# Kernel tuning notes

Measured on AMD Instinct MI355X. Metric: run time of the kernel, lower is better.

Reference implementation:

```python
import jax, jax.numpy as jnp
import numpy as np

W = 4           # cp_size (simulated ranks)
NUM_HEADS = 32
HEAD_SIZE = 128
NUM_KV_HEADS = 8
BLOCK_SIZE = 16
NUM_BLOCKS = 1024
MAX_BLOCKS = 32
MAX_CTX = 512   # <= _PARTITION_SIZE so single-partition stats are exact
NUM_SEQS = 32
SCALE = 1.0 / np.sqrt(HEAD_SIZE)
NEG_INF = -1e30


def setup_inputs() -> dict:
    key = jax.random.key(0)
    k1, k2, k3, k4, k5 = jax.random.split(key, 5)
    query = jax.random.normal(k1, (NUM_SEQS, 1, NUM_HEADS * HEAD_SIZE), dtype=jnp.float32)
    # per-rank paged KV caches, layout [W, num_blocks, kv_heads, block_size, head_size]
    key_cache = jax.random.normal(k2, (W, NUM_BLOCKS, NUM_KV_HEADS, BLOCK_SIZE, HEAD_SIZE), dtype=jnp.float32)
    value_cache = jax.random.normal(k3, (W, NUM_BLOCKS, NUM_KV_HEADS, BLOCK_SIZE, HEAD_SIZE), dtype=jnp.float32)
    block_tables = jax.random.randint(k4, (W, NUM_SEQS, MAX_BLOCKS), 0, NUM_BLOCKS, dtype=jnp.int32)
    context_lens = jax.random.randint(k5, (W, NUM_SEQS), 1, MAX_CTX + 1, dtype=jnp.int32)
    return {"query": query, "key_cache": key_cache, "value_cache": value_cache,
            "block_tables": block_tables, "context_lens": context_lens}


def reference(query, key_cache, value_cache, block_tables, context_lens):
    B, L, _ = query.shape
    S = B * L                       # num_seqs (decode: L=1)
    G = NUM_KV_HEADS
    Q = NUM_HEADS // G              # queries per kv head
    T = MAX_BLOCKS * BLOCK_SIZE     # max context per rank

    q = query.reshape(S, G, Q, HEAD_SIZE)
    ridx = jnp.arange(W)[:, None, None]
    # gather paged blocks: [W, S, MAX_BLOCKS, G, BLOCK_SIZE, D] -> [W, S, G, T, D]
    k = key_cache[ridx, block_tables].transpose(0, 1, 3, 2, 4, 5).reshape(W, S, G, T, HEAD_SIZE)
    v = value_cache[ridx, block_tables].transpose(0, 1, 3, 2, 4, 5).reshape(W, S, G, T, HEAD_SIZE)

    logits = jnp.einsum('sgqd,wsgtd->wsgqt', q, k) * SCALE
    mask = jnp.arange(T)[None, None, None, None, :] < context_lens[:, :, None, None, None]
    logits = jnp.where(mask, logits, NEG_INF)

    # per-rank online-softmax stats (== paged_attention_v2 single-partition output)
    m = jnp.max(logits, axis=-1)                      # [W,S,G,Q] max logit per rank
    p = jnp.exp(logits - m[..., None])
    p = jnp.where(mask, p, 0.0)
    esum = jnp.sum(p, axis=-1)                        # [W,S,G,Q]
    out_r = jnp.einsum('wsgqt,wsgtd->wsgqd', p, v) / esum[..., None]  # normalized per-rank out

    # cross-rank log-sum-exp reduction (distributed_paged_attention_v2_reduce)
    gmax = jnp.max(m, axis=0)                         # [S,G,Q]
    w_r = esum * jnp.exp(m - gmax[None])              # [W,S,G,Q]
    out = jnp.sum(out_r * w_r[..., None], axis=0) / jnp.sum(w_r, axis=0)[..., None]

    return out.reshape(B, L, NUM_HEADS * HEAD_SIZE)
```

## Files before the change

### kernel.cpp

```cpp
#include <hip/hip_runtime.h>
#include <math.h>

#define W 4
#define NUM_HEADS 32
#define HEAD_SIZE 128
#define G 8
#define QPG 4
#define BLOCK_SZ 16
#define NUM_BLOCKS 1024
#define MAX_BLOCKS 32
#define S 32
#define SPLIT 2
#define NPART (W * SPLIT)
#define SCALE 0.08838834764831845f
#define NEG_BIG (-1e30f)

#define BLK_STRIDE (G * BLOCK_SZ * HEAD_SIZE)
#define WG_STRIDE  (NUM_BLOCKS * BLK_STRIDE)

__global__ __launch_bounds__(256, 5)
void pa_partial_kernel(const float* __restrict__ query,
                       const float* __restrict__ key_cache,
                       const float* __restrict__ value_cache,
                       const int* __restrict__ block_tables,
                       const int* __restrict__ context_lens,
                       float* __restrict__ acc_ws,
                       float* __restrict__ m_ws,
                       float* __restrict__ e_ws)
{
    int bx = blockIdx.x;
    const int p = bx % SPLIT; bx /= SPLIT;
    const int g = bx % G;     bx /= G;
    const int s = bx % S;
    const int w = bx / S;

    const int tid   = threadIdx.x;
    const int accid = tid >> 5;
    const int lane  = tid & 31;
    const int d0    = lane * 4;
    const int h     = accid + 8 * p;

    __shared__ int   bt_lds[MAX_BLOCKS];
    __shared__ float sm_m[8][QPG];
    __shared__ float sm_e[8][QPG];
    __shared__ float sm_acc[8][QPG][HEAD_SIZE];

    if (tid < MAX_BLOCKS)
        bt_lds[tid] = block_tables[((size_t)w * S + s) * MAX_BLOCKS + tid];
    __syncthreads();

    float4 qf[QPG];
#pragma unroll
    for (int qi = 0; qi < QPG; ++qi)
        qf[qi] = *reinterpret_cast<const float4*>(
            query + ((size_t)s * NUM_HEADS + g * QPG + qi) * HEAD_SIZE + d0);

    const int ctx = context_lens[w * S + s];
    const float* kbase = key_cache   + (size_t)w * WG_STRIDE + (size_t)g * BLOCK_SZ * HEAD_SIZE;
    const float* vbase = value_cache + (size_t)w * WG_STRIDE + (size_t)g * BLOCK_SZ * HEAD_SIZE;

    float  m_i[QPG], e_i[QPG];
    float4 acc[QPG];
#pragma unroll
    for (int qi = 0; qi < QPG; ++qi) {
        m_i[qi] = NEG_BIG; e_i[qi] = 0.f;
        acc[qi] = make_float4(0.f, 0.f, 0.f, 0.f);
    }

    for (int t = h; t < ctx; t += 2 * 16) {
        const int off1 = bt_lds[t >> 4] * BLK_STRIDE + (t & 15) * HEAD_SIZE + d0;
        const float4 k1 = *reinterpret_cast<const float4*>(kbase + off1);
        const float4 v1 = *reinterpret_cast<const float4*>(vbase + off1);
        const int  t2   = t + 16;
        const bool vld2 = t2 < ctx;
        float4 k2 = make_float4(0.f, 0.f, 0.f, 0.f);
        float4 v2 = make_float4(0.f, 0.f, 0.f, 0.f);
        if (vld2) {
            const int off2 = bt_lds[t2 >> 4] * BLK_STRIDE + (t2 & 15) * HEAD_SIZE + d0;
            k2 = *reinterpret_cast<const float4*>(kbase + off2);
            v2 = *reinterpret_cast<const float4*>(vbase + off2);
        }

        float4 dv1, dv2;
        dv1.x = qf[0].x*k1.x + qf[0].y*k1.y + qf[0].z*k1.z + qf[0].w*k1.w;
        dv1.y = qf[1].x*k1.x + qf[1].y*k1.y + qf[1].z*k1.z + qf[1].w*k1.w;
        dv1.z = qf[2].x*k1.x + qf[2].y*k1.y + qf[2].z*k1.z + qf[2].w*k1.w;
        dv1.w = qf[3].x*k1.x + qf[3].y*k1.y + qf[3].z*k1.z + qf[3].w*k1.w;
        dv2.x = qf[0].x*k2.x + qf[0].y*k2.y + qf[0].z*k2.z + qf[0].w*k2.w;
        dv2.y = qf[1].x*k2.x + qf[1].y*k2.y + qf[1].z*k2.z + qf[1].w*k2.w;
        dv2.z = qf[2].x*k2.x + qf[2].y*k2.y + qf[2].z*k2.z + qf[2].w*k2.w;
        dv2.w = qf[3].x*k2.x + qf[3].y*k2.y + qf[3].z*k2.z + qf[3].w*k2.w;
#pragma unroll
        for (int o = 16; o > 0; o >>= 1) {
            dv1.x += __shfl_xor(dv1.x, o); dv1.y += __shfl_xor(dv1.y, o);
            dv1.z += __shfl_xor(dv1.z, o); dv1.w += __shfl_xor(dv1.w, o);
            dv2.x += __shfl_xor(dv2.x, o); dv2.y += __shfl_xor(dv2.y, o);
            dv2.z += __shfl_xor(dv2.z, o); dv2.w += __shfl_xor(dv2.w, o);
        }
        const float l1[QPG] = {dv1.x*SCALE, dv1.y*SCALE, dv1.z*SCALE, dv1.w*SCALE};
        float l2[QPG] = {dv2.x*SCALE, dv2.y*SCALE, dv2.z*SCALE, dv2.w*SCALE};
#pragma unroll
        for (int qi = 0; qi < QPG; ++qi) if (!vld2) l2[qi] = NEG_BIG;

#pragma unroll
        for (int qi = 0; qi < QPG; ++qi) {
            const float mn    = fmaxf(m_i[qi], fmaxf(l1[qi], l2[qi]));
            const float alpha = __expf(m_i[qi] - mn);
            const float p1    = __expf(l1[qi] - mn);
            const float p2    = __expf(l2[qi] - mn);
            m_i[qi] = mn;
            e_i[qi] = e_i[qi] * alpha + (p1 + p2);
            acc[qi].x = fmaf(acc[qi].x, alpha, fmaf(p1, v1.x, p2 * v2.x));
            acc[qi].y = fmaf(acc[qi].y, alpha, fmaf(p1, v1.y, p2 * v2.y));
            acc[qi].z = fmaf(acc[qi].z, alpha, fmaf(p1, v1.z, p2 * v2.z));
            acc[qi].w = fmaf(acc[qi].w, alpha, fmaf(p1, v1.w, p2 * v2.w));
        }
    }

#pragma unroll
    for (int qi = 0; qi < QPG; ++qi) {
        if (lane == 0) { sm_m[accid][qi] = m_i[qi]; sm_e[accid][qi] = e_i[qi]; }
        sm_acc[accid][qi][d0 + 0] = acc[qi].x;
        sm_acc[accid][qi][d0 + 1] = acc[qi].y;
        sm_acc[accid][qi][d0 + 2] = acc[qi].z;
        sm_acc[accid][qi][d0 + 3] = acc[qi].w;
    }
    __syncthreads();

    const int r = w * SPLIT + p;
    for (int pi = tid; pi < QPG * HEAD_SIZE; pi += 256) {
        const int qi = pi >> 7;
        const int d  = pi & (HEAD_SIZE - 1);
        float gm = NEG_BIG;
#pragma unroll
        for (int hh = 0; hh < 8; ++hh) gm = fmaxf(gm, sm_m[hh][qi]);
        float num = 0.f, den = 0.f;
#pragma unroll
        for (int hh = 0; hh < 8; ++hh) {
            const float sc = __expf(sm_m[hh][qi] - gm);
            num += sm_acc[hh][qi][d] * sc;
            den += sm_e[hh][qi] * sc;
        }
        const size_t idx = (((size_t)r * S + s) * G + g) * QPG + qi;
        acc_ws[idx * HEAD_SIZE + d] = num;
        if (d == 0) { m_ws[idx] = gm; e_ws[idx] = den; }
    }
}

__global__ __launch_bounds__(256)
void pa_reduce_kernel(const float* __restrict__ acc_ws,
                      const float* __restrict__ m_ws,
                      const float* __restrict__ e_ws,
                      float* __restrict__ out)
{
    const int bx = blockIdx.x;
    const int s = bx / G, g = bx % G;
    const int tid = threadIdx.x;
    for (int pi = tid; pi < QPG * HEAD_SIZE; pi += 256) {
        const int qi = pi >> 7;
        const int d  = pi & (HEAD_SIZE - 1);
        float mw[NPART], ew[NPART];
        float gm = NEG_BIG;
#pragma unroll
        for (int r = 0; r < NPART; ++r) {
            const size_t idx = (((size_t)r * S + s) * G + g) * QPG + qi;
            mw[r] = m_ws[idx];
            ew[r] = e_ws[idx];
            gm = fmaxf(gm, mw[r]);
        }
        float num = 0.f, den = 0.f;
#pragma unroll
        for (int r = 0; r < NPART; ++r) {
            const float sc = __expf(mw[r] - gm);
            const size_t idx = (((size_t)r * S + s) * G + g) * QPG + qi;
            num += acc_ws[idx * HEAD_SIZE + d] * sc;
            den += ew[r] * sc;
        }
        out[((size_t)s * NUM_HEADS + g * QPG + qi) * HEAD_SIZE + d] = num / den;
    }
}

__global__ __launch_bounds__(256)
void pa_fused_kernel(const float* __restrict__ query,
                     const float* __restrict__ key_cache,
                     const float* __restrict__ value_cache,
                     const int* __restrict__ block_tables,
                     const int* __restrict__ context_lens,
                     float* __restrict__ out)
{
    const int bx = blockIdx.x;
    const int s = bx / G, g = bx % G;
    const int tid   = threadIdx.x;
    const int accid = tid >> 5;
    const int lane  = tid & 31;
    const int d0    = lane * 4;

    __shared__ int   bt_lds[MAX_BLOCKS];
    __shared__ float sm_m[8][QPG];
    __shared__ float sm_e[8][QPG];
    __shared__ float sm_acc[8][QPG][HEAD_SIZE];

    float4 qf[QPG];
#pragma unroll
    for (int qi = 0; qi < QPG; ++qi)
        qf[qi] = *reinterpret_cast<const float4*>(
            query + ((size_t)s * NUM_HEADS + g * QPG + qi) * HEAD_SIZE + d0);

    float  m_i[QPG], e_i[QPG];
    float4 acc[QPG];
#pragma unroll
    for (int qi = 0; qi < QPG; ++qi) {
        m_i[qi] = NEG_BIG; e_i[qi] = 0.f;
        acc[qi] = make_float4(0.f, 0.f, 0.f, 0.f);
    }

    for (int w = 0; w < W; ++w) {
        __syncthreads();
        if (tid < MAX_BLOCKS)
            bt_lds[tid] = block_tables[((size_t)w * S + s) * MAX_BLOCKS + tid];
        __syncthreads();
        const int ctx = context_lens[w * S + s];
        const float* kbase = key_cache   + (size_t)w * WG_STRIDE + (size_t)g * BLOCK_SZ * HEAD_SIZE;
        const float* vbase = value_cache + (size_t)w * WG_STRIDE + (size_t)g * BLOCK_SZ * HEAD_SIZE;
        for (int t = accid; t < ctx; t += 8) {
            const int off = bt_lds[t >> 4] * BLK_STRIDE + (t & 15) * HEAD_SIZE + d0;
            const float4 kx = *reinterpret_cast<const float4*>(kbase + off);
            const float4 vx = *reinterpret_cast<const float4*>(vbase + off);
            float4 dv;
            dv.x = qf[0].x*kx.x + qf[0].y*kx.y + qf[0].z*kx.z + qf[0].w*kx.w;
            dv.y = qf[1].x*kx.x + qf[1].y*kx.y + qf[1].z*kx.z + qf[1].w*kx.w;
            dv.z = qf[2].x*kx.x + qf[2].y*kx.y + qf[2].z*kx.z + qf[2].w*kx.w;
            dv.w = qf[3].x*kx.x + qf[3].y*kx.y + qf[3].z*kx.z + qf[3].w*kx.w;
#pragma unroll
            for (int o = 16; o > 0; o >>= 1) {
                dv.x += __shfl_xor(dv.x, o); dv.y += __shfl_xor(dv.y, o);
                dv.z += __shfl_xor(dv.z, o); dv.w += __shfl_xor(dv.w, o);
            }
            const float lg[QPG] = {dv.x*SCALE, dv.y*SCALE, dv.z*SCALE, dv.w*SCALE};
#pragma unroll
            for (int qi = 0; qi < QPG; ++qi) {
                const float mn    = fmaxf(m_i[qi], lg[qi]);
                const float alpha = __expf(m_i[qi] - mn);
                const float pp    = __expf(lg[qi] - mn);
                m_i[qi] = mn;
                e_i[qi] = e_i[qi] * alpha + pp;
                acc[qi].x = fmaf(acc[qi].x, alpha, pp * vx.x);
                acc[qi].y = fmaf(acc[qi].y, alpha, pp * vx.y);
                acc[qi].z = fmaf(acc[qi].z, alpha, pp * vx.z);
                acc[qi].w = fmaf(acc[qi].w, alpha, pp * vx.w);
            }
        }
    }

#pragma unroll
    for (int qi = 0; qi < QPG; ++qi) {
        if (lane == 0) { sm_m[accid][qi] = m_i[qi]; sm_e[accid][qi] = e_i[qi]; }
        sm_acc[accid][qi][d0 + 0] = acc[qi].x;
        sm_acc[accid][qi][d0 + 1] = acc[qi].y;
        sm_acc[accid][qi][d0 + 2] = acc[qi].z;
        sm_acc[accid][qi][d0 + 3] = acc[qi].w;
    }
    __syncthreads();

    for (int pi = tid; pi < QPG * HEAD_SIZE; pi += 256) {
        const int qi = pi >> 7;
        const int d  = pi & (HEAD_SIZE - 1);
        float gm = NEG_BIG;
#pragma unroll
        for (int hh = 0; hh < 8; ++hh) gm = fmaxf(gm, sm_m[hh][qi]);
        float num = 0.f, den = 0.f;
#pragma unroll
        for (int hh = 0; hh < 8; ++hh) {
            const float sc = __expf(sm_m[hh][qi] - gm);
            num += sm_acc[hh][qi][d] * sc;
            den += sm_e[hh][qi] * sc;
        }
        out[((size_t)s * NUM_HEADS + g * QPG + qi) * HEAD_SIZE + d] = num / den;
    }
}

extern "C" void kernel_launch(void* const* d_in, const int* in_sizes, int n_in,
                              void* d_out, int out_size, void* d_ws, size_t ws_size,
                              hipStream_t stream) {
    const float* query        = (const float*)d_in[0];
    const float* key_cache    = (const float*)d_in[1];
    const float* value_cache  = (const float*)d_in[2];
    const int*   block_tables = (const int*)d_in[3];
    const int*   context_lens = (const int*)d_in[4];
    float* out = (float*)d_out;

    const size_t n_acc   = (size_t)NPART * S * G * QPG * HEAD_SIZE;
    const size_t n_stats = (size_t)NPART * S * G * QPG;
    const size_t need    = (n_acc + 2 * n_stats) * sizeof(float);

    if (ws_size >= need) {
        float* acc_ws = (float*)d_ws;
        float* m_ws   = acc_ws + n_acc;
        float* e_ws   = m_ws + n_stats;
        pa_partial_kernel<<<W * S * G * SPLIT, 256, 0, stream>>>(
            query, key_cache, value_cache, block_tables, context_lens,
            acc_ws, m_ws, e_ws);
        pa_reduce_kernel<<<S * G, 256, 0, stream>>>(acc_ws, m_ws, e_ws, out);
    } else {
        pa_fused_kernel<<<S * G, 256, 0, stream>>>(
            query, key_cache, value_cache, block_tables, context_lens, out);
    }
}
```

Before: 463.7 us.

## Double-buffer KV chunks in LDS via async global_load_lds in partial kernel

The partial attention kernel now stages each 16-token KV block for its head into shared memory with the asynchronous global-to-LDS load builtin, double-buffered so the next block's load overlaps compute on the current one. Partition assignment changes from interleaved tokens to interleaved whole blocks per split, and the accumulator scratch reuses the staging buffer. This aims to hide global load latency and issue wider coalesced loads, at the cost of more LDS (32KB), a barrier per chunk, and occupancy lowered from 5 to 4 blocks per CU.

```diff
diff --git a/kernel.cpp b/kernel.cpp
--- a/kernel.cpp
+++ b/kernel.cpp
@@ -1,5 +1,6 @@
 #include <hip/hip_runtime.h>
 #include <math.h>
+#include <stdint.h>
 
 #define W 4
 #define NUM_HEADS 32
@@ -16,9 +17,27 @@
 #define NEG_BIG (-1e30f)
 
 #define BLK_STRIDE (G * BLOCK_SZ * HEAD_SIZE)
-#define WG_STRIDE  (NUM_BLOCKS * BLK_STRIDE)
-
-__global__ __launch_bounds__(256, 5)
+#define WG_STRIDE  ((size_t)NUM_BLOCKS * BLK_STRIDE)
+#define CHUNK_ELEMS (BLOCK_SZ * HEAD_SIZE)
+
+typedef const __attribute__((address_space(1))) uint32_t* gas_ptr;
+typedef __attribute__((address_space(3))) uint32_t* las_ptr;
+
+__device__ __forceinline__ void stage_chunk(const float* __restrict__ ksrc,
+                                            const float* __restrict__ vsrc,
+                                            float* kv_dst, int tid)
+{
+    const int wv = tid >> 6;
+    const int ln = tid & 63;
+    const int b0 = wv * 512;
+    const int b1 = b0 + 256;
+    __builtin_amdgcn_global_load_lds((gas_ptr)(ksrc + b0 + ln * 4), (las_ptr)(kv_dst + b0),               16, 0, 0);
+    __builtin_amdgcn_global_load_lds((gas_ptr)(ksrc + b1 + ln * 4), (las_ptr)(kv_dst + b1),               16, 0, 0);
+    __builtin_amdgcn_global_load_lds((gas_ptr)(vsrc + b0 + ln * 4), (las_ptr)(kv_dst + CHUNK_ELEMS + b0), 16, 0, 0);
+    __builtin_amdgcn_global_load_lds((gas_ptr)(vsrc + b1 + ln * 4), (las_ptr)(kv_dst + CHUNK_ELEMS + b1), 16, 0, 0);
+}
+
+__global__ __launch_bounds__(256, 4)
 void pa_partial_kernel(const float* __restrict__ query,
                        const float* __restrict__ key_cache,
                        const float* __restrict__ value_cache,
@@ -29,8 +48,8 @@
                        float* __restrict__ e_ws)
 {
     int bx = blockIdx.x;
-    const int p = bx % SPLIT; bx /= SPLIT;
-    const int g = bx % G;     bx /= G;
+    const int p = bx & 1; bx >>= 1;
+    const int g = bx % G; bx /= G;
     const int s = bx % S;
     const int w = bx / S;
 
@@ -38,16 +57,16 @@
     const int accid = tid >> 5;
     const int lane  = tid & 31;
     const int d0    = lane * 4;
-    const int h     = accid + 8 * p;
-
-    __shared__ int   bt_lds[MAX_BLOCKS];
-    __shared__ float sm_m[8][QPG];
-    __shared__ float sm_e[8][QPG];
-    __shared__ float sm_acc[8][QPG][HEAD_SIZE];
-
-    if (tid < MAX_BLOCKS)
-        bt_lds[tid] = block_tables[((size_t)w * S + s) * MAX_BLOCKS + tid];
-    __syncthreads();
+
+    __shared__ float smem[2 * 2 * CHUNK_ELEMS];
+    __shared__ float sm_m[8][QPG], sm_e[8][QPG];
+
+    const int ctx    = context_lens[w * S + s];
+    const int nc_all = (ctx + BLOCK_SZ - 1) >> 4;
+    const int cnt    = (nc_all - p + 1) >> 1;
+    const int* bt = block_tables + ((size_t)w * S + s) * MAX_BLOCKS;
+    const float* kbase = key_cache   + (size_t)w * WG_STRIDE + (size_t)g * CHUNK_ELEMS;
+    const float* vbase = value_cache + (size_t)w * WG_STRIDE + (size_t)g * CHUNK_ELEMS;
 
     float4 qf[QPG];
 #pragma unroll
@@ -55,10 +74,6 @@
         qf[qi] = *reinterpret_cast<const float4*>(
             query + ((size_t)s * NUM_HEADS + g * QPG + qi) * HEAD_SIZE + d0);
 
-    const int ctx = context_lens[w * S + s];
-    const float* kbase = key_cache   + (size_t)w * WG_STRIDE + (size_t)g * BLOCK_SZ * HEAD_SIZE;
-    const float* vbase = value_cache + (size_t)w * WG_STRIDE + (size_t)g * BLOCK_SZ * HEAD_SIZE;
-
     float  m_i[QPG], e_i[QPG];
     float4 acc[QPG];
 #pragma unroll
@@ -67,63 +82,77 @@
         acc[qi] = make_float4(0.f, 0.f, 0.f, 0.f);
     }
 
-    for (int t = h; t < ctx; t += 2 * 16) {
-        const int off1 = bt_lds[t >> 4] * BLK_STRIDE + (t & 15) * HEAD_SIZE + d0;
-        const float4 k1 = *reinterpret_cast<const float4*>(kbase + off1);
-        const float4 v1 = *reinterpret_cast<const float4*>(vbase + off1);
-        const int  t2   = t + 16;
-        const bool vld2 = t2 < ctx;
-        float4 k2 = make_float4(0.f, 0.f, 0.f, 0.f);
-        float4 v2 = make_float4(0.f, 0.f, 0.f, 0.f);
-        if (vld2) {
-            const int off2 = bt_lds[t2 >> 4] * BLK_STRIDE + (t2 & 15) * HEAD_SIZE + d0;
-            k2 = *reinterpret_cast<const float4*>(kbase + off2);
-            v2 = *reinterpret_cast<const float4*>(vbase + off2);
-        }
-
-        float4 dv1, dv2;
-        dv1.x = qf[0].x*k1.x + qf[0].y*k1.y + qf[0].z*k1.z + qf[0].w*k1.w;
-        dv1.y = qf[1].x*k1.x + qf[1].y*k1.y + qf[1].z*k1.z + qf[1].w*k1.w;
-        dv1.z = qf[2].x*k1.x + qf[2].y*k1.y + qf[2].z*k1.z + qf[2].w*k1.w;
-        dv1.w = qf[3].x*k1.x + qf[3].y*k1.y + qf[3].z*k1.z + qf[3].w*k1.w;
-        dv2.x = qf[0].x*k2.x + qf[0].y*k2.y + qf[0].z*k2.z + qf[0].w*k2.w;
-        dv2.y = qf[1].x*k2.x + qf[1].y*k2.y + qf[1].z*k2.z + qf[1].w*k2.w;
-        dv2.z = qf[2].x*k2.x + qf[2].y*k2.y + qf[2].z*k2.z + qf[2].w*k2.w;
-        dv2.w = qf[3].x*k2.x + qf[3].y*k2.y + qf[3].z*k2.z + qf[3].w*k2.w;
-#pragma unroll
-        for (int o = 16; o > 0; o >>= 1) {
-            dv1.x += __shfl_xor(dv1.x, o); dv1.y += __shfl_xor(dv1.y, o);
-            dv1.z += __shfl_xor(dv1.z, o); dv1.w += __shfl_xor(dv1.w, o);
-            dv2.x += __shfl_xor(dv2.x, o); dv2.y += __shfl_xor(dv2.y, o);
-            dv2.z += __shfl_xor(dv2.z, o); dv2.w += __shfl_xor(dv2.w, o);
-        }
-        const float l1[QPG] = {dv1.x*SCALE, dv1.y*SCALE, dv1.z*SCALE, dv1.w*SCALE};
-        float l2[QPG] = {dv2.x*SCALE, dv2.y*SCALE, dv2.z*SCALE, dv2.w*SCALE};
-#pragma unroll
-        for (int qi = 0; qi < QPG; ++qi) if (!vld2) l2[qi] = NEG_BIG;
-
-#pragma unroll
-        for (int qi = 0; qi < QPG; ++qi) {
-            const float mn    = fmaxf(m_i[qi], fmaxf(l1[qi], l2[qi]));
-            const float alpha = __expf(m_i[qi] - mn);
-            const float p1    = __expf(l1[qi] - mn);
-            const float p2    = __expf(l2[qi] - mn);
-            m_i[qi] = mn;
-            e_i[qi] = e_i[qi] * alpha + (p1 + p2);
-            acc[qi].x = fmaf(acc[qi].x, alpha, fmaf(p1, v1.x, p2 * v2.x));
-            acc[qi].y = fmaf(acc[qi].y, alpha, fmaf(p1, v1.y, p2 * v2.y));
-            acc[qi].z = fmaf(acc[qi].z, alpha, fmaf(p1, v1.z, p2 * v2.z));
-            acc[qi].w = fmaf(acc[qi].w, alpha, fmaf(p1, v1.w, p2 * v2.w));
-        }
-    }
-
+    if (cnt > 0) {
+        const size_t bb = (size_t)bt[p] * BLK_STRIDE;
+        stage_chunk(kbase + bb, vbase + bb, smem, tid);
+    }
+    __syncthreads();
+
+    int buf = 0;
+    for (int i = 0; i < cnt; ++i) {
+        const int c = p + 2 * i;
+        if (i + 1 < cnt) {
+            const size_t bb = (size_t)bt[c + 2] * BLK_STRIDE;
+            stage_chunk(kbase + bb, vbase + bb, smem + (buf ^ 1) * (2 * CHUNK_ELEMS), tid);
+        }
+
+        const float* kb = smem + buf * (2 * CHUNK_ELEMS);
+        const float* vb = kb + CHUNK_ELEMS;
+        const int gt0 = (c << 4) + accid;
+        if (gt0 < ctx) {
+            const float4 k1 = *reinterpret_cast<const float4*>(kb + accid * HEAD_SIZE + d0);
+            const float4 v1 = *reinterpret_cast<const float4*>(vb + accid * HEAD_SIZE + d0);
+            const float4 k2 = *reinterpret_cast<const float4*>(kb + (accid + 8) * HEAD_SIZE + d0);
+            const float4 v2 = *reinterpret_cast<const float4*>(vb + (accid + 8) * HEAD_SIZE + d0);
+
+            float4 dv1, dv2;
+            dv1.x = qf[0].x*k1.x + qf[0].y*k1.y + qf[0].z*k1.z + qf[0].w*k1.w;
+            dv1.y = qf[1].x*k1.x + qf[1].y*k1.y + qf[1].z*k1.z + qf[1].w*k1.w;
+            dv1.z = qf[2].x*k1.x + qf[2].y*k1.y + qf[2].z*k1.z + qf[2].w*k1.w;
+            dv1.w = qf[3].x*k1.x + qf[3].y*k1.y + qf[3].z*k1.z + qf[3].w*k1.w;
+            dv2.x = qf[0].x*k2.x + qf[0].y*k2.y + qf[0].z*k2.z + qf[0].w*k2.w;
+            dv2.y = qf[1].x*k2.x + qf[1].y*k2.y + qf[1].z*k2.z + qf[1].w*k2.w;
+            dv2.z = qf[2].x*k2.x + qf[2].y*k2.y + qf[2].z*k2.z + qf[2].w*k2.w;
+            dv2.w = qf[3].x*k2.x + qf[3].y*k2.y + qf[3].z*k2.z + qf[3].w*k2.w;
+#pragma unroll
+            for (int o = 16; o > 0; o >>= 1) {
+                dv1.x += __shfl_xor(dv1.x, o); dv1.y += __shfl_xor(dv1.y, o);
+                dv1.z += __shfl_xor(dv1.z, o); dv1.w += __shfl_xor(dv1.w, o);
+                dv2.x += __shfl_xor(dv2.x, o); dv2.y += __shfl_xor(dv2.y, o);
+                dv2.z += __shfl_xor(dv2.z, o); dv2.w += __shfl_xor(dv2.w, o);
+            }
+            const float l1[QPG] = {dv1.x*SCALE, dv1.y*SCALE, dv1.z*SCALE, dv1.w*SCALE};
+            float l2[QPG] = {dv2.x*SCALE, dv2.y*SCALE, dv2.z*SCALE, dv2.w*SCALE};
+            const bool vld2 = (gt0 + 8) < ctx;
+#pragma unroll
+            for (int qi = 0; qi < QPG; ++qi) if (!vld2) l2[qi] = NEG_BIG;
+
+#pragma unroll
+            for (int qi = 0; qi < QPG; ++qi) {
+                const float mn    = fmaxf(m_i[qi], fmaxf(l1[qi], l2[qi]));
+                const float alpha = __expf(m_i[qi] - mn);
+                const float p1    = __expf(l1[qi] - mn);
+                const float p2    = __expf(l2[qi] - mn);
+                m_i[qi] = mn;
+                e_i[qi] = e_i[qi] * alpha + (p1 + p2);
+                acc[qi].x = fmaf(acc[qi].x, alpha, fmaf(p1, v1.x, p2 * v2.x));
+                acc[qi].y = fmaf(acc[qi].y, alpha, fmaf(p1, v1.y, p2 * v2.y));
+                acc[qi].z = fmaf(acc[qi].z, alpha, fmaf(p1, v1.z, p2 * v2.z));
+                acc[qi].w = fmaf(acc[qi].w, alpha, fmaf(p1, v1.w, p2 * v2.w));
+            }
+        }
+        __syncthreads();
+        buf ^= 1;
+    }
+
+    float* sacc = smem;
 #pragma unroll
     for (int qi = 0; qi < QPG; ++qi) {
         if (lane == 0) { sm_m[accid][qi] = m_i[qi]; sm_e[accid][qi] = e_i[qi]; }
-        sm_acc[accid][qi][d0 + 0] = acc[qi].x;
-        sm_acc[accid][qi][d0 + 1] = acc[qi].y;
-        sm_acc[accid][qi][d0 + 2] = acc[qi].z;
-        sm_acc[accid][qi][d0 + 3] = acc[qi].w;
+        sacc[accid * 512 + qi * 128 + d0 + 0] = acc[qi].x;
+        sacc[accid * 512 + qi * 128 + d0 + 1] = acc[qi].y;
+        sacc[accid * 512 + qi * 128 + d0 + 2] = acc[qi].z;
+        sacc[accid * 512 + qi * 128 + d0 + 3] = acc[qi].w;
     }
     __syncthreads();
 
@@ -138,7 +167,7 @@
 #pragma unroll
         for (int hh = 0; hh < 8; ++hh) {
             const float sc = __expf(sm_m[hh][qi] - gm);
-            num += sm_acc[hh][qi][d] * sc;
+            num += sacc[hh * 512 + qi * 128 + d] * sc;
             den += sm_e[hh][qi] * sc;
         }
         const size_t idx = (((size_t)r * S + s) * G + g) * QPG + qi;
@@ -220,8 +249,8 @@
             bt_lds[tid] = block_tables[((size_t)w * S + s) * MAX_BLOCKS + tid];
         __syncthreads();
         const int ctx = context_lens[w * S + s];
-        const float* kbase = key_cache   + (size_t)w * WG_STRIDE + (size_t)g * BLOCK_SZ * HEAD_SIZE;
-        const float* vbase = value_cache + (size_t)w * WG_STRIDE + (size_t)g * BLOCK_SZ * HEAD_SIZE;
+        const float* kbase = key_cache   + (size_t)w * WG_STRIDE + (size_t)g * CHUNK_ELEMS;
+        const float* vbase = value_cache + (size_t)w * WG_STRIDE + (size_t)g * CHUNK_ELEMS;
         for (int t = accid; t < ctx; t += 8) {
             const int off = bt_lds[t >> 4] * BLK_STRIDE + (t & 15) * HEAD_SIZE + d0;
             const float4 kx = *reinterpret_cast<const float4*>(kbase + off);
```

Result: no change. 466.4 us (+0.6%).
